# Kernel tuning notes

Hardware: AMD Instinct MI355X
Metric: run time of the kernel (lower is better)

## Reference

```python
import jax, jax.numpy as jnp
import numpy as np

N_NODES = 100_000
N_EDGES = 1_600_000
IN_C, OUT_C = 128, 64


def setup_inputs() -> dict:
    key = jax.random.key(0)
    k1, k2, k3, k4 = jax.random.split(key, 4)
    x = jax.random.normal(k1, (N_NODES, IN_C), dtype=jnp.float32)
    # xavier_uniform with relu gain sqrt(2)
    gain = float(np.sqrt(2.0))
    bound = gain * float(np.sqrt(6.0 / (IN_C + OUT_C)))
    weight = jax.random.uniform(k2, (IN_C, OUT_C), minval=-bound, maxval=bound, dtype=jnp.float32)
    bias = jnp.zeros((OUT_C,), dtype=jnp.float32)
    src = jax.random.randint(k3, (N_EDGES,), 0, N_NODES, dtype=jnp.int32)
    dst = jax.random.randint(k4, (N_EDGES,), 0, N_NODES, dtype=jnp.int32)
    return {"x": x, "weight": weight, "bias": bias, "src": src, "dst": dst}


def reference(x, weight, bias, src, dst):
    # DGL GraphConv, norm='both'.
    n = x.shape[0]
    ones = jnp.ones(src.shape, dtype=x.dtype)
    deg_out = jax.ops.segment_sum(ones, src, num_segments=n)  # source out-degree
    deg_in = jax.ops.segment_sum(ones, dst, num_segments=n)   # destination in-degree
    norm_src = jnp.maximum(deg_out, 1.0) ** -0.5
    norm_dst = jnp.maximum(deg_in, 1.0) ** -0.5
    h = x * norm_src[:, None]          # [N, IN]
    # in_channels > out_channels: apply weight before aggregation (DGL fast path)
    h = h @ weight                      # [N, OUT]
    msg = h[src]                        # [E, OUT] gather
    agg = jax.ops.segment_sum(msg, dst, num_segments=n)  # [N, OUT] scatter-add
    return agg * norm_dst[:, None] + bias
```

## Files before the change

kernel.cpp:

```cpp
#include <hip/hip_runtime.h>
#include <hip/hip_bf16.h>

#define N_NODES 100000
#define N_EDGES 1600000
#define IN_C    128
#define OUT_C   64

#define REC_W 48
#define CAP   47

typedef __bf16 bf16x8 __attribute__((ext_vector_type(8)));
typedef float  f32x4  __attribute__((ext_vector_type(4)));

#define DEGS_OFF  0
#define REC_OFF   400000
#define H_OFF     19600000

__global__ __launch_bounds__(256) void fill_kernel(
    const int* __restrict__ src, const int* __restrict__ dst,
    int* __restrict__ degs, int* __restrict__ rec) {
  int i = blockIdx.x * 256 + threadIdx.x;
  if (i < N_EDGES) {
    int s = src[i];
    int d = dst[i];
    atomicAdd(&degs[s], 1);
    int pos = atomicAdd(&rec[d * REC_W], 1);
    if (pos < CAP) rec[d * REC_W + 1 + pos] = s;
  }
}

__global__ __launch_bounds__(256) void gemm_kernel(
    const float* __restrict__ x, const float* __restrict__ w,
    const int* __restrict__ degs, __bf16* __restrict__ h, int n_groups) {
  const int lane = threadIdx.x & 63;
  const int l15 = lane & 15;
  const int q = lane >> 4;
  const int wave = blockIdx.x * (blockDim.x >> 6) + (threadIdx.x >> 6);
  const int n_waves = gridDim.x * (blockDim.x >> 6);

  bf16x8 bfrag[4][4];
#pragma unroll
  for (int kc = 0; kc < 4; ++kc) {
#pragma unroll
    for (int t = 0; t < 4; ++t) {
      bf16x8 tmp;
#pragma unroll
      for (int j = 0; j < 8; ++j)
        tmp[j] = (__bf16)w[(kc * 32 + q * 8 + j) * OUT_C + t * 16 + l15];
      bfrag[kc][t] = tmp;
    }
  }

  for (int g = wave; g < n_groups; g += n_waves) {
    const int n0 = g * 16;
    const float* xp = x + (long)(n0 + l15) * IN_C + q * 8;

    f32x4 acc[4];
#pragma unroll
    for (int t = 0; t < 4; ++t) {
      f32x4 z = {0.f, 0.f, 0.f, 0.f};
      acc[t] = z;
    }

#pragma unroll
    for (int kc = 0; kc < 4; ++kc) {
      f32x4 u = *(const f32x4*)(xp + kc * 32);
      f32x4 v = *(const f32x4*)(xp + kc * 32 + 4);
      bf16x8 a;
#pragma unroll
      for (int j = 0; j < 4; ++j) {
        a[j] = (__bf16)u[j];
        a[4 + j] = (__bf16)v[j];
      }
#pragma unroll
      for (int t = 0; t < 4; ++t)
        acc[t] = __builtin_amdgcn_mfma_f32_16x16x32_bf16(a, bfrag[kc][t], acc[t], 0, 0, 0);
    }

#pragma unroll
    for (int r = 0; r < 4; ++r) {
      const int row = n0 + q * 4 + r;
      int dg = degs[row];
      float fs = (float)(dg < 1 ? 1 : dg);
      const float s = rsqrtf(fs);
#pragma unroll
      for (int t = 0; t < 4; ++t)
        h[(long)row * OUT_C + t * 16 + l15] = (__bf16)(acc[t][r] * s);
    }
  }
}

__global__ __launch_bounds__(256) void aggregate_kernel(
    const __bf16* __restrict__ h, const int* __restrict__ rec,
    const float* __restrict__ bias, float* __restrict__ out) {
  const int node = blockIdx.x * 4 + (threadIdx.x >> 6);
  if (node >= N_NODES) return;
  const int lane = threadIdx.x & 63;
  const int* rn = rec + node * REC_W;
  int cnt = rn[0];
  float fd = (float)(cnt < 1 ? 1 : cnt);
  const float ndv = rsqrtf(fd);
  int end = cnt < CAP ? cnt : CAP;

  float a0 = 0.f, a1 = 0.f, a2 = 0.f, a3 = 0.f;
  int j = 0;
  for (; j + 4 <= end; j += 4) {
    int s0 = rn[1 + j];
    int s1 = rn[2 + j];
    int s2 = rn[3 + j];
    int s3 = rn[4 + j];
    a0 += (float)h[(long)s0 * OUT_C + lane];
    a1 += (float)h[(long)s1 * OUT_C + lane];
    a2 += (float)h[(long)s2 * OUT_C + lane];
    a3 += (float)h[(long)s3 * OUT_C + lane];
  }
  for (; j < end; ++j) a0 += (float)h[(long)rn[1 + j] * OUT_C + lane];

  float r = ((a0 + a1) + (a2 + a3)) * ndv + bias[lane];
  out[(long)node * OUT_C + lane] = r;
}

extern "C" void kernel_launch(void* const* d_in, const int* in_sizes, int n_in,
                              void* d_out, int out_size, void* d_ws, size_t ws_size,
                              hipStream_t stream) {
  const float* x    = (const float*)d_in[0];
  const float* w    = (const float*)d_in[1];
  const float* bias = (const float*)d_in[2];
  const int*   src  = (const int*)d_in[3];
  const int*   dst  = (const int*)d_in[4];
  float* out = (float*)d_out;

  char* ws = (char*)d_ws;
  int*    degs = (int*)(ws + DEGS_OFF);
  int*    rec  = (int*)(ws + REC_OFF);
  __bf16* h    = (__bf16*)(ws + H_OFF);

  hipMemsetAsync(ws, 0, (size_t)REC_OFF + (size_t)N_NODES * REC_W * sizeof(int), stream);

  fill_kernel<<<(N_EDGES + 255) / 256, 256, 0, stream>>>(src, dst, degs, rec);

  const int n_groups = N_NODES / 16;
  gemm_kernel<<<256, 256, 0, stream>>>(x, w, degs, h, n_groups);

  aggregate_kernel<<<(N_NODES + 3) / 4, 256, 0, stream>>>(h, rec, bias, out);
}
```

Before: 305.1 us.

## Fuse edge fill with GEMM and move source norm into aggregation

```diff
diff --git a/kernel.cpp b/kernel.cpp
--- a/kernel.cpp
+++ b/kernel.cpp
@@ -6,37 +6,43 @@
 #define IN_C    128
 #define OUT_C   64
 
-#define REC_W 48
-#define CAP   47
+#define SLOT_W 48
+#define CAP    47
+
+#define GEMM_BLK 512
+#define FILL_BLK ((N_EDGES + 255) / 256)
 
 typedef __bf16 bf16x8 __attribute__((ext_vector_type(8)));
 typedef float  f32x4  __attribute__((ext_vector_type(4)));
 
 #define DEGS_OFF  0
-#define REC_OFF   400000
-#define H_OFF     19600000
+#define CNT_OFF   400000
+#define SLOT_OFF  800000
+#define H_OFF     20000000
 
-__global__ __launch_bounds__(256) void fill_kernel(
+__global__ __launch_bounds__(256) void fused_fill_gemm(
+    const float* __restrict__ x, const float* __restrict__ w,
     const int* __restrict__ src, const int* __restrict__ dst,
-    int* __restrict__ degs, int* __restrict__ rec) {
-  int i = blockIdx.x * 256 + threadIdx.x;
-  if (i < N_EDGES) {
-    int s = src[i];
-    int d = dst[i];
-    atomicAdd(&degs[s], 1);
-    int pos = atomicAdd(&rec[d * REC_W], 1);
-    if (pos < CAP) rec[d * REC_W + 1 + pos] = s;
+    int* __restrict__ degs, int* __restrict__ cnt, int* __restrict__ slots,
+    __bf16* __restrict__ h) {
+  if (blockIdx.x >= GEMM_BLK) {
+    const int i = (blockIdx.x - GEMM_BLK) * 256 + threadIdx.x;
+    if (i < N_EDGES) {
+      const int s = src[i];
+      const int d = dst[i];
+      atomicAdd(&degs[s], 1);
+      const int pos = atomicAdd(&cnt[d], 1);
+      if (pos < CAP) slots[d * SLOT_W + pos] = s;
+    }
+    return;
   }
-}
 
-__global__ __launch_bounds__(256) void gemm_kernel(
-    const float* __restrict__ x, const float* __restrict__ w,
-    const int* __restrict__ degs, __bf16* __restrict__ h, int n_groups) {
   const int lane = threadIdx.x & 63;
   const int l15 = lane & 15;
   const int q = lane >> 4;
-  const int wave = blockIdx.x * (blockDim.x >> 6) + (threadIdx.x >> 6);
-  const int n_waves = gridDim.x * (blockDim.x >> 6);
+  const int wave = blockIdx.x * 4 + (threadIdx.x >> 6);
+  const int n_waves = GEMM_BLK * 4;
+  const int n_groups = N_NODES / 16;
 
   bf16x8 bfrag[4][4];
 #pragma unroll
@@ -80,41 +86,47 @@
 #pragma unroll
     for (int r = 0; r < 4; ++r) {
       const int row = n0 + q * 4 + r;
-      int dg = degs[row];
-      float fs = (float)(dg < 1 ? 1 : dg);
-      const float s = rsqrtf(fs);
 #pragma unroll
       for (int t = 0; t < 4; ++t)
-        h[(long)row * OUT_C + t * 16 + l15] = (__bf16)(acc[t][r] * s);
+        h[(long)row * OUT_C + t * 16 + l15] = (__bf16)acc[t][r];
     }
   }
 }
 
 __global__ __launch_bounds__(256) void aggregate_kernel(
-    const __bf16* __restrict__ h, const int* __restrict__ rec,
+    const __bf16* __restrict__ h, const int* __restrict__ cnt,
+    const int* __restrict__ slots, const int* __restrict__ degs,
     const float* __restrict__ bias, float* __restrict__ out) {
   const int node = blockIdx.x * 4 + (threadIdx.x >> 6);
   if (node >= N_NODES) return;
   const int lane = threadIdx.x & 63;
-  const int* rn = rec + node * REC_W;
-  int cnt = rn[0];
-  float fd = (float)(cnt < 1 ? 1 : cnt);
-  const float ndv = rsqrtf(fd);
-  int end = cnt < CAP ? cnt : CAP;
+  const int c = cnt[node];
+  const float ndv = rsqrtf((float)(c < 1 ? 1 : c));
+  const int end = c < CAP ? c : CAP;
+  const int* sl = slots + (long)node * SLOT_W;
 
   float a0 = 0.f, a1 = 0.f, a2 = 0.f, a3 = 0.f;
   int j = 0;
   for (; j + 4 <= end; j += 4) {
-    int s0 = rn[1 + j];
-    int s1 = rn[2 + j];
-    int s2 = rn[3 + j];
-    int s3 = rn[4 + j];
-    a0 += (float)h[(long)s0 * OUT_C + lane];
-    a1 += (float)h[(long)s1 * OUT_C + lane];
-    a2 += (float)h[(long)s2 * OUT_C + lane];
-    a3 += (float)h[(long)s3 * OUT_C + lane];
+    int s0 = sl[j];
+    int s1 = sl[j + 1];
+    int s2 = sl[j + 2];
+    int s3 = sl[j + 3];
+    int d0 = degs[s0], d1 = degs[s1], d2 = degs[s2], d3 = degs[s3];
+    float w0 = rsqrtf((float)(d0 < 1 ? 1 : d0));
+    float w1 = rsqrtf((float)(d1 < 1 ? 1 : d1));
+    float w2 = rsqrtf((float)(d2 < 1 ? 1 : d2));
+    float w3 = rsqrtf((float)(d3 < 1 ? 1 : d3));
+    a0 += (float)h[(long)s0 * OUT_C + lane] * w0;
+    a1 += (float)h[(long)s1 * OUT_C + lane] * w1;
+    a2 += (float)h[(long)s2 * OUT_C + lane] * w2;
+    a3 += (float)h[(long)s3 * OUT_C + lane] * w3;
   }
-  for (; j < end; ++j) a0 += (float)h[(long)rn[1 + j] * OUT_C + lane];
+  for (; j < end; ++j) {
+    int s0 = sl[j];
+    int d0 = degs[s0];
+    a0 += (float)h[(long)s0 * OUT_C + lane] * rsqrtf((float)(d0 < 1 ? 1 : d0));
+  }
 
   float r = ((a0 + a1) + (a2 + a3)) * ndv + bias[lane];
   out[(long)node * OUT_C + lane] = r;
@@ -131,16 +143,16 @@
   float* out = (float*)d_out;
 
   char* ws = (char*)d_ws;
-  int*    degs = (int*)(ws + DEGS_OFF);
-  int*    rec  = (int*)(ws + REC_OFF);
-  __bf16* h    = (__bf16*)(ws + H_OFF);
+  int*    degs  = (int*)(ws + DEGS_OFF);
+  int*    cnt   = (int*)(ws + CNT_OFF);
+  int*    slots = (int*)(ws + SLOT_OFF);
+  __bf16* h     = (__bf16*)(ws + H_OFF);
 
-  hipMemsetAsync(ws, 0, (size_t)REC_OFF + (size_t)N_NODES * REC_W * sizeof(int), stream);
+  hipMemsetAsync(ws, 0, 2 * N_NODES * sizeof(int), stream);
 
-  fill_kernel<<<(N_EDGES + 255) / 256, 256, 0, stream>>>(src, dst, degs, rec);
+  fused_fill_gemm<<<GEMM_BLK + FILL_BLK, 256, 0, stream>>>(
+      x, w, src, dst, degs, cnt, slots, h);
 
-  const int n_groups = N_NODES / 16;
-  gemm_kernel<<<256, 256, 0, stream>>>(x, w, degs, h, n_groups);
-
-  aggregate_kernel<<<(N_NODES + 3) / 4, 256, 0, stream>>>(h, rec, bias, out);
+  aggregate_kernel<<<(N_NODES + 3) / 4, 256, 0, stream>>>(
+      h, cnt, slots, degs, bias, out);
 }
```

Measured after the change: 324.1 us. 1.06x slower.
